# Kernel optimization log

Measured on AMD Instinct MI355X. Metric: run time of the kernel, lower is better.

The kernel has to match this reference:

```python
import jax, jax.numpy as jnp
import numpy as np

B, S, D = 8, 1024, 768
H = 12            # atten_heads
DH = D // H       # head dim = 64
F = 3072          # liner_dim
EPS = 1e-6


def _layer_norm(x, gamma, beta):
    mu = jnp.mean(x, axis=-1, keepdims=True)
    var = jnp.mean(jnp.square(x - mu), axis=-1, keepdims=True)
    return (x - mu) * jax.lax.rsqrt(var + EPS) * gamma + beta


def setup_inputs() -> dict:
    key = jax.random.key(0)
    ks = jax.random.split(key, 12)
    s = 0.02
    return {
        "x": jax.random.normal(ks[0], (B, S, D), jnp.float32),
        "Wq": jax.random.normal(ks[1], (D, D), jnp.float32) * s,
        "bq": jnp.zeros((D,), jnp.float32),
        "Wk": jax.random.normal(ks[2], (D, D), jnp.float32) * s,
        "bk": jnp.zeros((D,), jnp.float32),
        "Wv": jax.random.normal(ks[3], (D, D), jnp.float32) * s,
        "bv": jnp.zeros((D,), jnp.float32),
        "Wo": jax.random.normal(ks[4], (D, D), jnp.float32) * s,
        "bo": jnp.zeros((D,), jnp.float32),
        "g1": jnp.ones((D,), jnp.float32),
        "beta1": jnp.zeros((D,), jnp.float32),
        "g2": jnp.ones((D,), jnp.float32),
        "beta2": jnp.zeros((D,), jnp.float32),
        "W1": jax.random.normal(ks[5], (D, F), jnp.float32) * s,
        "b1": jnp.zeros((F,), jnp.float32),
        "W2": jax.random.normal(ks[6], (F, D), jnp.float32) * s,
        "b2": jnp.zeros((D,), jnp.float32),
    }


def reference(x, Wq, bq, Wk, bk, Wv, bv, Wo, bo, g1, beta1, g2, beta2, W1, b1, W2, b2):
    # pre-LN
    h = _layer_norm(x, g1, beta1)                       # [B,S,D]
    # QKV projections; tf.split(axis=-1)+concat(axis=0) == per-head view
    q = (h @ Wq + bq).reshape(B, S, H, DH)
    k = (h @ Wk + bk).reshape(B, S, H, DH)
    v = (h @ Wv + bv).reshape(B, S, H, DH)
    scale = 1.0 / jnp.sqrt(jnp.float32(DH))
    scores = jnp.einsum('bqhd,bkhd->bhqk', q, k) * scale  # [B,H,S,S]
    attn = jax.nn.softmax(scores, axis=-1)
    ctx = jnp.einsum('bhqk,bkhd->bqhd', attn, v).reshape(B, S, D)
    attn_out = ctx @ Wo + bo
    x2 = attn_out + x                                    # residual (dropout=0 at eval)
    # MLP block with exact (erf) GELU, as keras.activations.gelu default
    y = _layer_norm(x2, g2, beta2)
    y = jax.nn.gelu(y @ W1 + b1, approximate=False)
    y = y @ W2 + b2
    return x2 + y
```

## Files before the change

### kernel.cpp

```cpp
#include <hip/hip_runtime.h>
#include <stdint.h>

__device__ __forceinline__ float b2f(uint16_t u) {
    union { uint32_t i; float f; } v; v.i = ((uint32_t)u) << 16; return v.f;
}
__device__ __forceinline__ float b2f_lo(uint32_t u) {
    union { uint32_t i; float f; } v; v.i = u << 16; return v.f;
}
__device__ __forceinline__ float b2f_hi(uint32_t u) {
    union { uint32_t i; float f; } v; v.i = u & 0xFFFF0000u; return v.f;
}
__device__ __forceinline__ uint16_t f2b(float f) {
    union { float f; uint32_t i; } v; v.f = f;
    uint32_t r = v.i + 0x7FFF + ((v.i >> 16) & 1);
    return (uint16_t)(r >> 16);
}

typedef short  fragAB __attribute__((ext_vector_type(8)));
typedef float  fragC  __attribute__((ext_vector_type(4)));

#define MFMA(a, b, c) __builtin_amdgcn_mfma_f32_16x16x32_bf16((a), (b), (c), 0, 0, 0)

__device__ __forceinline__ void gload_lds16(const uint16_t* g, uint16_t* l) {
    __builtin_amdgcn_global_load_lds(
        (const __attribute__((address_space(1))) void*)g,
        (__attribute__((address_space(3))) void*)l, 16, 0, 0);
}

__global__ void detect_kernel(const uint16_t* __restrict__ g1, int* __restrict__ flag) {
    if (threadIdx.x == 0 && blockIdx.x == 0)
        flag[0] = (g1[0] == 0x3F80) ? 0 : 1;
}

__global__ __launch_bounds__(256) void convert_small_kernel(
    const void* p0, const void* p1, const void* p2, const void* p3, const void* p4,
    const void* p5, const void* p6, const void* p7, const void* p8, const void* p9,
    uint16_t* __restrict__ out, const int* __restrict__ flag)
{
    const int f = *flag;
    const void* p; int n; int off;
    switch (blockIdx.x) {
        case 0: p = p0; n = 768;  off = 0;    break;
        case 1: p = p1; n = 768;  off = 768;  break;
        case 2: p = p2; n = 768;  off = 1536; break;
        case 3: p = p3; n = 768;  off = 2304; break;
        case 4: p = p4; n = 768;  off = 3072; break;
        case 5: p = p5; n = 768;  off = 3840; break;
        case 6: p = p6; n = 768;  off = 4608; break;
        case 7: p = p7; n = 768;  off = 5376; break;
        case 8: p = p8; n = 3072; off = 6144; break;
        default: p = p9; n = 768; off = 9216; break;
    }
    uint16_t* o = out + off;
    for (int i = threadIdx.x; i < n; i += 256)
        o[i] = f ? f2b(((const float*)p)[i]) : ((const uint16_t*)p)[i];
}

__global__ __launch_bounds__(256) void transpose_kernel(
    const void* __restrict__ in, uint16_t* __restrict__ out, int R, int C,
    const int* __restrict__ flag)
{
    __shared__ uint16_t tile[32][33];
    const int f  = *flag;
    const int tx = threadIdx.x & 31;
    const int ty = threadIdx.x >> 5;
    const int r0 = blockIdx.y * 32, c0 = blockIdx.x * 32;
    #pragma unroll
    for (int i = 0; i < 32; i += 8) {
        size_t idx = (size_t)(r0 + ty + i) * C + c0 + tx;
        tile[ty + i][tx] = f ? f2b(((const float*)in)[idx]) : ((const uint16_t*)in)[idx];
    }
    __syncthreads();
    #pragma unroll
    for (int i = 0; i < 32; i += 8)
        out[(size_t)(c0 + ty + i) * R + r0 + tx] = tile[tx][ty + i];
}

__global__ __launch_bounds__(256) void convert_ln_kernel(
    const void* __restrict__ xraw, const int* __restrict__ flag,
    const uint16_t* __restrict__ g, const uint16_t* __restrict__ beta,
    uint16_t* __restrict__ xb, uint16_t* __restrict__ out)
{
    const int lane = threadIdx.x & 63;
    const int wave = threadIdx.x >> 6;
    const int row  = blockIdx.x * 4 + wave;
    uint32_t* xrow = (uint32_t*)(xb + (size_t)row * 768);
    float v[12];
    if (*flag) {
        const float2* xr = (const float2*)((const float*)xraw + (size_t)row * 768);
        #pragma unroll
        for (int i = 0; i < 6; i++) {
            float2 t = xr[i * 64 + lane];
            uint16_t a = f2b(t.x), b = f2b(t.y);
            xrow[i * 64 + lane] = (uint32_t)a | ((uint32_t)b << 16);
            v[2 * i] = b2f(a); v[2 * i + 1] = b2f(b);
        }
    } else {
        const uint32_t* xr = (const uint32_t*)xraw + (size_t)row * 384;
        #pragma unroll
        for (int i = 0; i < 6; i++) {
            uint32_t u = xr[i * 64 + lane];
            xrow[i * 64 + lane] = u;
            v[2 * i] = b2f_lo(u); v[2 * i + 1] = b2f_hi(u);
        }
    }
    float sum = 0.f, sq = 0.f;
    #pragma unroll
    for (int j = 0; j < 12; j++) { sum += v[j]; sq += v[j] * v[j]; }
    #pragma unroll
    for (int off = 32; off > 0; off >>= 1) {
        sum += __shfl_xor(sum, off);
        sq  += __shfl_xor(sq, off);
    }
    const float invn = 1.0f / 768.0f;
    float mu  = sum * invn;
    float var = sq * invn - mu * mu;
    float rs  = rsqrtf(var + 1e-6f);
    uint32_t* orow = (uint32_t*)(out + (size_t)row * 768);
    const uint32_t* gp = (const uint32_t*)g;
    const uint32_t* bp = (const uint32_t*)beta;
    #pragma unroll
    for (int i = 0; i < 6; i++) {
        int p = i * 64 + lane;
        uint32_t gu = gp[p], bu = bp[p];
        float o0 = (v[2 * i]     - mu) * rs * b2f_lo(gu) + b2f_lo(bu);
        float o1 = (v[2 * i + 1] - mu) * rs * b2f_hi(gu) + b2f_hi(bu);
        orow[p] = (uint32_t)f2b(o0) | ((uint32_t)f2b(o1) << 16);
    }
}

__global__ __launch_bounds__(256) void finish_ln_kernel(
    const uint16_t* __restrict__ pa, const uint16_t* __restrict__ pb,
    const uint16_t* __restrict__ bias, const uint16_t* __restrict__ res,
    const uint16_t* __restrict__ g, const uint16_t* __restrict__ beta,
    uint16_t* __restrict__ x2, uint16_t* __restrict__ out)
{
    const int lane = threadIdx.x & 63;
    const int wave = threadIdx.x >> 6;
    const int row  = blockIdx.x * 4 + wave;
    const uint32_t* par = (const uint32_t*)pa  + (size_t)row * 384;
    const uint32_t* pbr = (const uint32_t*)pb  + (size_t)row * 384;
    const uint32_t* rr  = (const uint32_t*)res + (size_t)row * 384;
    const uint32_t* bb  = (const uint32_t*)bias;
    uint32_t* x2r = (uint32_t*)(x2 + (size_t)row * 768);
    float v[12];
    float sum = 0.f, sq = 0.f;
    #pragma unroll
    for (int i = 0; i < 6; i++) {
        int p = i * 64 + lane;
        uint32_t ua = par[p], ub = pbr[p], ur = rr[p], uc = bb[p];
        float s0 = b2f_lo(ua) + b2f_lo(ub) + b2f_lo(uc) + b2f_lo(ur);
        float s1 = b2f_hi(ua) + b2f_hi(ub) + b2f_hi(uc) + b2f_hi(ur);
        uint16_t q0 = f2b(s0), q1 = f2b(s1);
        x2r[p] = (uint32_t)q0 | ((uint32_t)q1 << 16);
        float a = b2f(q0), b = b2f(q1);
        v[2 * i] = a; v[2 * i + 1] = b;
        sum += a + b; sq += a * a + b * b;
    }
    #pragma unroll
    for (int off = 32; off > 0; off >>= 1) {
        sum += __shfl_xor(sum, off);
        sq  += __shfl_xor(sq, off);
    }
    const float invn = 1.0f / 768.0f;
    float mu  = sum * invn;
    float var = sq * invn - mu * mu;
    float rs  = rsqrtf(var + 1e-6f);
    uint32_t* orow = (uint32_t*)(out + (size_t)row * 768);
    const uint32_t* gp = (const uint32_t*)g;
    const uint32_t* bp = (const uint32_t*)beta;
    #pragma unroll
    for (int i = 0; i < 6; i++) {
        int p = i * 64 + lane;
        uint32_t gu = gp[p], bu = bp[p];
        float o0 = (v[2 * i]     - mu) * rs * b2f_lo(gu) + b2f_lo(bu);
        float o1 = (v[2 * i + 1] - mu) * rs * b2f_hi(gu) + b2f_hi(bu);
        orow[p] = (uint32_t)f2b(o0) | ((uint32_t)f2b(o1) << 16);
    }
}

__global__ __launch_bounds__(256) void gemm_kernel(
    const uint16_t* __restrict__ A, const uint16_t* __restrict__ Wt,
    const uint16_t* __restrict__ bias, uint16_t* __restrict__ out,
    uint16_t* __restrict__ outB, int M, int N, int K, int mode)
{
    __shared__ __align__(16) uint16_t As[128 * 32];
    __shared__ __align__(16) uint16_t Bs[128 * 32];
    __shared__ __align__(16) uint16_t Es[4 * 1152];
    const int tid  = threadIdx.x;
    const int lane = tid & 63;
    const int wave = tid >> 6;
    const int wm   = (wave >> 1) * 64;
    const int wn   = (wave & 1) * 64;
    const int qrow = lane & 15;
    const int quad = lane >> 4;

    const int gx = gridDim.x, gy = gridDim.y, gz = gridDim.z;
    const int flat = blockIdx.x + gx * (blockIdx.y + gy * blockIdx.z);
    const int xcd = flat & 7;
    const int local = flat >> 3;
    const int n0 = (local % gx) * 128;
    const int mz = (local / gx) * 8 + xcd;
    const int m0 = (mz % gy) * 128;
    const int slice = mz / gy;
    const int kLen = K / gz;
    const int kOff = slice * kLen;

    const int srow = lane >> 2;
    const int pcol = lane & 3;

    fragC acc[4][4] = {};

    for (int k0 = kOff; k0 < kOff + kLen; k0 += 32) {
        __syncthreads();
        #pragma unroll
        for (int j = 0; j < 2; j++) {
            const int rbase = (j * 4 + wave) * 16;
            const int r = rbase + srow;
            const int g = (pcol - (r >> 1)) & 3;
            const uint16_t* ga = A  + (size_t)(m0 + r) * K + k0 + g * 8;
            const uint16_t* gb = Wt + (size_t)(n0 + r) * K + k0 + g * 8;
            gload_lds16(ga, &As[rbase * 32]);
            gload_lds16(gb, &Bs[rbase * 32]);
        }
        __syncthreads();
        fragAB af[4], bf[4];
        #pragma unroll
        for (int t = 0; t < 4; t++) {
            const int ra = wm + t * 16 + qrow;
            const int rb = wn + t * 16 + qrow;
            const int ca = (quad + (ra >> 1)) & 3;
            const int cb = (quad + (rb >> 1)) & 3;
            af[t] = *(const fragAB*)&As[ra * 32 + ca * 8];
            bf[t] = *(const fragAB*)&Bs[rb * 32 + cb * 8];
        }
        #pragma unroll
        for (int mi = 0; mi < 4; mi++)
            #pragma unroll
            for (int ni = 0; ni < 4; ni++)
                acc[mi][ni] = MFMA(af[mi], bf[ni], acc[mi][ni]);
    }

    uint16_t* po = (mode == 7 && slice) ? outB : out;
    uint16_t* eb = &Es[wave * 1152];
    float bvv[4];
    if (mode != 7) {
        #pragma unroll
        for (int ni = 0; ni < 4; ni++) bvv[ni] = b2f(bias[n0 + wn + ni * 16 + qrow]);
    }
    const int er = lane >> 2, ec = (lane & 3) * 16;
    #pragma unroll
    for (int mi = 0; mi < 4; mi++) {
        #pragma unroll
        for (int ni = 0; ni < 4; ni++) {
            #pragma unroll
            for (int r = 0; r < 4; r++) {
                float v = acc[mi][ni][r];
                if (mode != 7) {
                    v += bvv[ni];
                    if (mode == 2) {
                        float arg = v * (1.5957691216f + 0.0713548163f * v * v);
                        v = v * __builtin_amdgcn_rcpf(1.0f + __expf(-arg));
                    }
                }
                eb[(quad * 4 + r) * 72 + ni * 16 + qrow] = f2b(v);
            }
        }
        __asm__ volatile("s_waitcnt lgkmcnt(0)" ::: "memory");
        uint16_t* dst = po + (size_t)(m0 + wm + mi * 16 + er) * N + n0 + wn + ec;
        *(int4*)dst       = *(const int4*)&eb[er * 72 + ec];
        *(int4*)(dst + 8) = *(const int4*)&eb[er * 72 + ec + 8];
        __asm__ volatile("" ::: "memory");
    }
}

__global__ __launch_bounds__(256) void finish_kernel(
    const uint16_t* __restrict__ pa, const uint16_t* __restrict__ pb,
    const uint16_t* __restrict__ bias, const uint16_t* __restrict__ res,
    void* __restrict__ out, const int* __restrict__ flag)
{
    const int i = (blockIdx.x * 256 + threadIdx.x) * 4;
    const int n = i % 768;
    ushort4 av = *(const ushort4*)(pa + i);
    ushort4 pv = *(const ushort4*)(pb + i);
    ushort4 rv = *(const ushort4*)(res + i);
    ushort4 cv = *(const ushort4*)(bias + n);
    float o0 = b2f(av.x) + b2f(pv.x) + b2f(cv.x) + b2f(rv.x);
    float o1 = b2f(av.y) + b2f(pv.y) + b2f(cv.y) + b2f(rv.y);
    float o2 = b2f(av.z) + b2f(pv.z) + b2f(cv.z) + b2f(rv.z);
    float o3 = b2f(av.w) + b2f(pv.w) + b2f(cv.w) + b2f(rv.w);
    if (flag && *flag) {
        *(float4*)((float*)out + i) = make_float4(o0, o1, o2, o3);
    } else {
        ushort4 ov;
        ov.x = f2b(o0); ov.y = f2b(o1); ov.z = f2b(o2); ov.w = f2b(o3);
        *(ushort4*)((uint16_t*)out + i) = ov;
    }
}

__global__ __launch_bounds__(256) void attn_kernel(
    const uint16_t* __restrict__ QKV, uint16_t* __restrict__ ctx)
{
    __shared__ __align__(16) uint16_t Ks[128 * 72];
    __shared__ __align__(16) uint16_t Vs[64 * 72];
    __shared__ __align__(16) uint16_t Ps[4][2][16 * 72];
    const int tid  = threadIdx.x;
    const int lane = tid & 63;
    const int wave = tid >> 6;
    const int qrow = lane & 15;
    const int quad = lane >> 4;

    const int flat = blockIdx.x + 8 * blockIdx.y;
    const int xcd = flat & 7, local = flat >> 3;
    const int bh = xcd * 12 + (local >> 3);
    const int b  = bh / 12, hh = bh % 12;
    const int q0blk = (local & 7) * 128;
    const int q0 = q0blk + wave * 32;

    const uint16_t* base = QKV + (size_t)b * 1024 * 2304;
    const uint16_t* Qp = base + hh * 64;
    const uint16_t* Kp = base + 768 + hh * 64;
    const uint16_t* Vp = base + 1536 + hh * 64;

    const int srow = tid >> 2;
    const int scol = (tid & 3) * 16;
    const int pkey = srow ^ scol;

    fragAB qf[2][2];
    #pragma unroll
    for (int qq = 0; qq < 2; qq++)
        #pragma unroll
        for (int c = 0; c < 2; c++)
            qf[qq][c] = *(const fragAB*)(Qp + (size_t)(q0 + qq * 16 + qrow) * 2304 + c * 32 + quad * 8);

    fragC ao[2][4] = {};
    float lsum[2][4] = {};

    for (int kk = 0; kk < 1024; kk += 64) {
        __syncthreads();
        *(int4*)&Ks[srow * 72 + scol]     = *(const int4*)(Kp + (size_t)(kk + srow) * 2304 + scol);
        *(int4*)&Ks[srow * 72 + scol + 8] = *(const int4*)(Kp + (size_t)(kk + srow) * 2304 + scol + 8);
        {
            union { int4 q[2]; uint16_t u[16]; } t;
            t.q[0] = *(const int4*)(Vp + (size_t)(kk + srow) * 2304 + scol);
            t.q[1] = *(const int4*)(Vp + (size_t)(kk + srow) * 2304 + scol + 8);
            #pragma unroll
            for (int j = 0; j < 16; j++)
                Vs[(scol + j) * 72 + pkey] = t.u[j];
        }
        __syncthreads();

        fragC sc[2][4] = {};
        #pragma unroll
        for (int g = 0; g < 4; g++) {
            fragAB kf0 = *(const fragAB*)&Ks[(g * 16 + qrow) * 72 + quad * 8];
            fragAB kf1 = *(const fragAB*)&Ks[(g * 16 + qrow) * 72 + 32 + quad * 8];
            #pragma unroll
            for (int qq = 0; qq < 2; qq++) {
                sc[qq][g] = MFMA(qf[qq][0], kf0, sc[qq][g]);
                sc[qq][g] = MFMA(qf[qq][1], kf1, sc[qq][g]);
            }
        }

        #pragma unroll
        for (int qq = 0; qq < 2; qq++)
            #pragma unroll
            for (int g = 0; g < 4; g++)
                #pragma unroll
                for (int r = 0; r < 4; r++) {
                    float p = __expf(fminf(sc[qq][g][r] * 0.125f, 20.0f));
                    lsum[qq][r] += p;
                    Ps[wave][qq][(quad * 4 + r) * 72 + g * 16 + qrow] = f2b(p);
                }
        __syncthreads();

        fragAB pf[2][2];
        #pragma unroll
        for (int qq = 0; qq < 2; qq++)
            #pragma unroll
            for (int c = 0; c < 2; c++)
                pf[qq][c] = *(const fragAB*)&Ps[wave][qq][qrow * 72 + c * 32 + quad * 8];

        #pragma unroll
        for (int f = 0; f < 4; f++) {
            fragAB vf0 = *(const fragAB*)&Vs[(f * 16 + qrow) * 72 + ((0 + quad * 8) ^ (f * 16))];
            fragAB vf1 = *(const fragAB*)&Vs[(f * 16 + qrow) * 72 + ((32 + quad * 8) ^ (f * 16))];
            #pragma unroll
            for (int qq = 0; qq < 2; qq++) {
                ao[qq][f] = MFMA(pf[qq][0], vf0, ao[qq][f]);
                ao[qq][f] = MFMA(pf[qq][1], vf1, ao[qq][f]);
            }
        }
    }

    float inv[2][4];
    #pragma unroll
    for (int qq = 0; qq < 2; qq++)
        #pragma unroll
        for (int r = 0; r < 4; r++) {
            float s = lsum[qq][r];
            #pragma unroll
            for (int off = 1; off < 16; off <<= 1) s += __shfl_xor(s, off);
            inv[qq][r] = 1.0f / s;
        }

    #pragma unroll
    for (int qq = 0; qq < 2; qq++)
        #pragma unroll
        for (int f = 0; f < 4; f++)
            #pragma unroll
            for (int r = 0; r < 4; r++)
                Ks[(wave * 32 + qq * 16 + quad * 4 + r) * 72 + f * 16 + qrow] =
                    f2b(ao[qq][f][r] * inv[qq][r]);
    __syncthreads();
    {
        const int row = tid >> 1, half = tid & 1;
        uint16_t* dst = ctx + (size_t)(b * 1024 + q0blk + row) * 768 + hh * 64 + half * 32;
        const uint16_t* src = &Ks[row * 72 + half * 32];
        *(int4*)dst        = *(const int4*)src;
        *(int4*)(dst + 8)  = *(const int4*)(src + 8);
        *(int4*)(dst + 16) = *(const int4*)(src + 16);
        *(int4*)(dst + 24) = *(const int4*)(src + 24);
    }
}

extern "C" void kernel_launch(void* const* d_in, const int* in_sizes, int n_in,
                              void* d_out, int out_size, void* d_ws, size_t ws_size,
                              hipStream_t stream)
{
    (void)in_sizes; (void)n_in; (void)out_size; (void)ws_size;
    const void* x_raw  = d_in[0];
    const void* Wq_raw = d_in[1];
    const void* bq_raw = d_in[2];
    const void* Wk_raw = d_in[3];
    const void* bk_raw = d_in[4];
    const void* Wv_raw = d_in[5];
    const void* bv_raw = d_in[6];
    const void* Wo_raw = d_in[7];
    const void* bo_raw = d_in[8];
    const void* g1_raw = d_in[9];
    const void* be1_raw= d_in[10];
    const void* g2_raw = d_in[11];
    const void* be2_raw= d_in[12];
    const void* W1_raw = d_in[13];
    const void* b1_raw = d_in[14];
    const void* W2_raw = d_in[15];
    const void* b2_raw = d_in[16];

    uint8_t* ws = (uint8_t*)d_ws;
    const size_t SZ = (size_t)8192 * 768 * 2;
    uint16_t* xb    = (uint16_t*)(ws);
    uint16_t* h1    = (uint16_t*)(ws + SZ);
    uint16_t* QKVb  = (uint16_t*)(ws + 2 * SZ);
    uint16_t* ctx   = (uint16_t*)(ws + 5 * SZ);
    uint16_t* pWa   = (uint16_t*)(ws + 2 * SZ);
    uint16_t* pWb   = (uint16_t*)(ws + SZ);
    uint16_t* x2    = (uint16_t*)(ws + 5 * SZ);
    uint16_t* ln2   = (uint16_t*)(ws + 6 * SZ);
    uint16_t* y1    = (uint16_t*)(ws);
    uint16_t* pMa   = (uint16_t*)(ws + 4 * SZ);
    uint16_t* pMb   = (uint16_t*)(ws + 6 * SZ);
    uint8_t*  wts   = ws + 7 * SZ;
    uint16_t* WqkvT = (uint16_t*)(wts);
    uint16_t* WoT   = (uint16_t*)(wts + 3 * 1179648);
    uint16_t* W1T   = (uint16_t*)(wts + 4 * 1179648);
    uint16_t* W2T   = (uint16_t*)(wts + 4 * 1179648 + 4718592);
    uint16_t* smallv = (uint16_t*)(wts + 4 * 1179648 + 2 * 4718592);
    int* flag = (int*)(wts + 4 * 1179648 + 2 * 4718592 + 9984 * 2);
    uint16_t* G1   = smallv + 0,    *BE1 = smallv + 768;
    uint16_t* G2   = smallv + 1536, *BE2 = smallv + 2304;
    uint16_t* BQKV = smallv + 3072;
    uint16_t* BO   = smallv + 5376;
    uint16_t* B1   = smallv + 6144, *B2 = smallv + 9216;

    dim3 blk(256);
    detect_kernel<<<1, 64, 0, stream>>>((const uint16_t*)g1_raw, flag);
    convert_small_kernel<<<10, blk, 0, stream>>>(g1_raw, be1_raw, g2_raw, be2_raw,
        bq_raw, bk_raw, bv_raw, bo_raw, b1_raw, b2_raw, smallv, flag);

    transpose_kernel<<<dim3(24, 24), blk, 0, stream>>>(Wq_raw, WqkvT,              768, 768, flag);
    transpose_kernel<<<dim3(24, 24), blk, 0, stream>>>(Wk_raw, WqkvT + 589824,     768, 768, flag);
    transpose_kernel<<<dim3(24, 24), blk, 0, stream>>>(Wv_raw, WqkvT + 2 * 589824, 768, 768, flag);
    transpose_kernel<<<dim3(24, 24), blk, 0, stream>>>(Wo_raw, WoT, 768, 768, flag);
    transpose_kernel<<<dim3(96, 24), blk, 0, stream>>>(W1_raw, W1T, 768, 3072, flag);
    transpose_kernel<<<dim3(24, 96), blk, 0, stream>>>(W2_raw, W2T, 3072, 768, flag);

    convert_ln_kernel<<<2048, blk, 0, stream>>>(x_raw, flag, G1, BE1, xb, h1);

    gemm_kernel<<<dim3(18, 64), blk, 0, stream>>>(h1, WqkvT, BQKV, QKVb, nullptr,
                                                  8192, 2304, 768, 0);

    attn_kernel<<<dim3(8, 96), blk, 0, stream>>>(QKVb, ctx);

    gemm_kernel<<<dim3(6, 64, 2), blk, 0, stream>>>(ctx, WoT, BO, pWa, pWb,
                                                    8192, 768, 768, 7);
    finish_ln_kernel<<<2048, blk, 0, stream>>>(pWa, pWb, BO, xb, G2, BE2, x2, ln2);

    gemm_kernel<<<dim3(24, 64), blk, 0, stream>>>(ln2, W1T, B1, y1, nullptr,
                                                  8192, 3072, 768, 2);

    gemm_kernel<<<dim3(6, 64, 2), blk, 0, stream>>>(y1, W2T, B2, pMa, pMb,
                                                    8192, 768, 3072, 7);
    finish_kernel<<<6144, blk, 0, stream>>>(pMa, pMb, B2, x2, d_out, flag);
}
```

Measured before the change: 325.3 us.

## Replace GEMM with 256x256-tile, 8-wave, 4-stage pipelined LDS kernel

Replaces the 128x128 single-buffered GEMM with a 256x256 tile kernel using 512 threads, a four-deep LDS ring of K-tiles filled with global_load_lds, and split-phase MFMA compute with priority raising and explicit barriers. The aim is to overlap global loads with MFMA work and raise arithmetic intensity per block. The XCD-aware block remapping and the LDS swizzle are dropped. The 128 KB LDS buffer limits occupancy, and the grids shrink a lot (e.g. 96 blocks for the Wo/W2 GEMMs per slice), which may underfill the device.

```diff
diff --git a/kernel.cpp b/kernel.cpp
--- a/kernel.cpp
+++ b/kernel.cpp
@@ -179,70 +179,118 @@
     }
 }
 
-__global__ __launch_bounds__(256) void gemm_kernel(
+__global__ __launch_bounds__(512, 2) void gemm256_kernel(
     const uint16_t* __restrict__ A, const uint16_t* __restrict__ Wt,
     const uint16_t* __restrict__ bias, uint16_t* __restrict__ out,
     uint16_t* __restrict__ outB, int M, int N, int K, int mode)
 {
-    __shared__ __align__(16) uint16_t As[128 * 32];
-    __shared__ __align__(16) uint16_t Bs[128 * 32];
-    __shared__ __align__(16) uint16_t Es[4 * 1152];
+    __shared__ __align__(16) uint16_t lds[65536];
+    uint16_t* ldsA = lds;
+    uint16_t* ldsB = lds + 32768;
+
     const int tid  = threadIdx.x;
     const int lane = tid & 63;
     const int wave = tid >> 6;
-    const int wm   = (wave >> 1) * 64;
-    const int wn   = (wave & 1) * 64;
     const int qrow = lane & 15;
     const int quad = lane >> 4;
-
-    const int gx = gridDim.x, gy = gridDim.y, gz = gridDim.z;
-    const int flat = blockIdx.x + gx * (blockIdx.y + gy * blockIdx.z);
-    const int xcd = flat & 7;
-    const int local = flat >> 3;
-    const int n0 = (local % gx) * 128;
-    const int mz = (local / gx) * 8 + xcd;
-    const int m0 = (mz % gy) * 128;
-    const int slice = mz / gy;
-    const int kLen = K / gz;
+    const int wm   = (wave >> 2) * 128;
+    const int wn   = (wave & 3) * 64;
+
+    const int m0 = blockIdx.y * 256;
+    const int n0 = blockIdx.x * 256;
+    const int slice = blockIdx.z;
+    const int kLen = K / gridDim.z;
     const int kOff = slice * kLen;
-
-    const int srow = lane >> 2;
-    const int pcol = lane & 3;
-
-    fragC acc[4][4] = {};
-
-    for (int k0 = kOff; k0 < kOff + kLen; k0 += 32) {
-        __syncthreads();
-        #pragma unroll
-        for (int j = 0; j < 2; j++) {
-            const int rbase = (j * 4 + wave) * 16;
-            const int r = rbase + srow;
-            const int g = (pcol - (r >> 1)) & 3;
-            const uint16_t* ga = A  + (size_t)(m0 + r) * K + k0 + g * 8;
-            const uint16_t* gb = Wt + (size_t)(n0 + r) * K + k0 + g * 8;
-            gload_lds16(ga, &As[rbase * 32]);
-            gload_lds16(gb, &Bs[rbase * 32]);
-        }
-        __syncthreads();
+    const int nt   = kLen >> 5;
+
+    const uint16_t* aS0 = A  + (size_t)(m0 + 32 * wave + (lane >> 2)) * K + kOff + (lane & 3) * 8;
+    const uint16_t* aS1 = aS0 + (size_t)16 * K;
+    const uint16_t* bS0 = Wt + (size_t)(n0 + 32 * wave + (lane >> 2)) * K + kOff + (lane & 3) * 8;
+    const uint16_t* bS1 = bS0 + (size_t)16 * K;
+    const int stOff = wave * 1024;
+    const int arOff = (wm + qrow) * 32 + quad * 8;
+    const int brOff = (wn + qrow) * 32 + quad * 8;
+
+    fragC acc[8][4] = {};
+
+    #pragma unroll
+    for (int tt = 0; tt < 3; ++tt) {
+        const int sb = tt * 8192 + stOff;
+        gload_lds16(aS0 + tt * 32, ldsA + sb);
+        gload_lds16(aS1 + tt * 32, ldsA + sb + 512);
+        gload_lds16(bS0 + tt * 32, ldsB + sb);
+        gload_lds16(bS1 + tt * 32, ldsB + sb + 512);
+    }
+    __asm__ volatile("s_waitcnt vmcnt(8)" ::: "memory");
+    __builtin_amdgcn_s_barrier();
+
+    auto tile = [&](int t, bool doStage, int ts) {
+        const int tb = (t & 3) * 8192;
+        const uint16_t* ar = ldsA + tb + arOff;
+        const uint16_t* br = ldsB + tb + brOff;
         fragAB af[4], bf[4];
         #pragma unroll
-        for (int t = 0; t < 4; t++) {
-            const int ra = wm + t * 16 + qrow;
-            const int rb = wn + t * 16 + qrow;
-            const int ca = (quad + (ra >> 1)) & 3;
-            const int cb = (quad + (rb >> 1)) & 3;
-            af[t] = *(const fragAB*)&As[ra * 32 + ca * 8];
-            bf[t] = *(const fragAB*)&Bs[rb * 32 + cb * 8];
-        }
-        #pragma unroll
-        for (int mi = 0; mi < 4; mi++)
-            #pragma unroll
-            for (int ni = 0; ni < 4; ni++)
-                acc[mi][ni] = MFMA(af[mi], bf[ni], acc[mi][ni]);
-    }
+        for (int m = 0; m < 4; m++) af[m] = *(const fragAB*)(ar + m * 512);
+        #pragma unroll
+        for (int n = 0; n < 4; n++) bf[n] = *(const fragAB*)(br + n * 512);
+        if (doStage) {
+            const int sb = (ts & 3) * 8192 + stOff;
+            gload_lds16(aS0 + ts * 32, ldsA + sb);
+            gload_lds16(aS1 + ts * 32, ldsA + sb + 512);
+        }
+        __builtin_amdgcn_s_barrier();
+        __asm__ volatile("s_waitcnt lgkmcnt(0)" ::: "memory");
+        __builtin_amdgcn_sched_barrier(0);
+        __builtin_amdgcn_s_setprio(1);
+        #pragma unroll
+        for (int m = 0; m < 4; m++)
+            #pragma unroll
+            for (int n = 0; n < 4; n++)
+                acc[m][n] = MFMA(af[m], bf[n], acc[m][n]);
+        __builtin_amdgcn_s_setprio(0);
+        __builtin_amdgcn_sched_barrier(0);
+        __builtin_amdgcn_s_barrier();
+        #pragma unroll
+        for (int m = 0; m < 4; m++) af[m] = *(const fragAB*)(ar + 2048 + m * 512);
+        if (doStage) {
+            const int sb = (ts & 3) * 8192 + stOff;
+            gload_lds16(bS0 + ts * 32, ldsB + sb);
+            gload_lds16(bS1 + ts * 32, ldsB + sb + 512);
+        }
+        __builtin_amdgcn_s_barrier();
+        __asm__ volatile("s_waitcnt lgkmcnt(0)" ::: "memory");
+        __builtin_amdgcn_sched_barrier(0);
+        __builtin_amdgcn_s_setprio(1);
+        #pragma unroll
+        for (int m = 0; m < 4; m++)
+            #pragma unroll
+            for (int n = 0; n < 4; n++)
+                acc[4 + m][n] = MFMA(af[m], bf[n], acc[4 + m][n]);
+        __builtin_amdgcn_s_setprio(0);
+        __builtin_amdgcn_sched_barrier(0);
+    };
+
+    int t = 0;
+    for (; t < nt - 3; ++t) {
+        tile(t, true, t + 3);
+        __asm__ volatile("s_waitcnt vmcnt(8)" ::: "memory");
+        __builtin_amdgcn_sched_barrier(0);
+        __builtin_amdgcn_s_barrier();
+    }
+    tile(t, false, 0);
+    __asm__ volatile("s_waitcnt vmcnt(4)" ::: "memory");
+    __builtin_amdgcn_s_barrier();
+    ++t;
+    tile(t, false, 0);
+    __asm__ volatile("s_waitcnt vmcnt(0)" ::: "memory");
+    __builtin_amdgcn_s_barrier();
+    ++t;
+    tile(t, false, 0);
+
+    __syncthreads();
 
     uint16_t* po = (mode == 7 && slice) ? outB : out;
-    uint16_t* eb = &Es[wave * 1152];
+    uint16_t* eb = lds + wave * 1152;
     float bvv[4];
     if (mode != 7) {
         #pragma unroll
@@ -250,7 +298,7 @@
     }
     const int er = lane >> 2, ec = (lane & 3) * 16;
     #pragma unroll
-    for (int mi = 0; mi < 4; mi++) {
+    for (int mi = 0; mi < 8; mi++) {
         #pragma unroll
         for (int ni = 0; ni < 4; ni++) {
             #pragma unroll
@@ -474,6 +522,7 @@
     uint16_t* B1   = smallv + 6144, *B2 = smallv + 9216;
 
     dim3 blk(256);
+    dim3 blk2(512);
     detect_kernel<<<1, 64, 0, stream>>>((const uint16_t*)g1_raw, flag);
     convert_small_kernel<<<10, blk, 0, stream>>>(g1_raw, be1_raw, g2_raw, be2_raw,
         bq_raw, bk_raw, bv_raw, bo_raw, b1_raw, b2_raw, smallv, flag);
@@ -487,19 +536,19 @@
 
     convert_ln_kernel<<<2048, blk, 0, stream>>>(x_raw, flag, G1, BE1, xb, h1);
 
-    gemm_kernel<<<dim3(18, 64), blk, 0, stream>>>(h1, WqkvT, BQKV, QKVb, nullptr,
-                                                  8192, 2304, 768, 0);
+    gemm256_kernel<<<dim3(9, 32), blk2, 0, stream>>>(h1, WqkvT, BQKV, QKVb, nullptr,
+                                                     8192, 2304, 768, 0);
 
     attn_kernel<<<dim3(8, 96), blk, 0, stream>>>(QKVb, ctx);
 
-    gemm_kernel<<<dim3(6, 64, 2), blk, 0, stream>>>(ctx, WoT, BO, pWa, pWb,
-                                                    8192, 768, 768, 7);
+    gemm256_kernel<<<dim3(3, 32, 2), blk2, 0, stream>>>(ctx, WoT, BO, pWa, pWb,
+                                                        8192, 768, 768, 7);
     finish_ln_kernel<<<2048, blk, 0, stream>>>(pWa, pWb, BO, xb, G2, BE2, x2, ln2);
 
-    gemm_kernel<<<dim3(24, 64), blk, 0, stream>>>(ln2, W1T, B1, y1, nullptr,
-                                                  8192, 3072, 768, 2);
-
-    gemm_kernel<<<dim3(6, 64, 2), blk, 0, stream>>>(y1, W2T, B2, pMa, pMb,
-                                                    8192, 768, 3072, 7);
+    gemm256_kernel<<<dim3(12, 32), blk2, 0, stream>>>(ln2, W1T, B1, y1, nullptr,
+                                                      8192, 3072, 768, 2);
+
+    gemm256_kernel<<<dim3(3, 32, 2), blk2, 0, stream>>>(y1, W2T, B2, pMa, pMb,
+                                                        8192, 768, 3072, 7);
     finish_kernel<<<6144, blk, 0, stream>>>(pMa, pMb, B2, x2, d_out, flag);
 }
```

Result: faster. 317.3 us (-2.5%).
